# Kernel tuning notes

Hardware: AMD Instinct MI355X
Metric: run time of the kernel (lower is better)

## Reference

```python
import jax, jax.numpy as jnp
import numpy as np

EPS = 1e-9

def dice(x, alpha):
    # Dice: batch-norm over dim 0 (unbiased var, ddof=1), then gated blend.
    mu = jnp.mean(x, axis=0)
    var = jnp.var(x, axis=0, ddof=1)
    p = jax.nn.sigmoid((x - mu) / jnp.sqrt(var + EPS))
    return alpha * x * (1.0 - p) + x * p


def setup_inputs() -> dict:
    key = jax.random.key(0)
    ks = jax.random.split(key, 8)
    bs, seq, dim = 2048, 200, 64
    d_in = dim * 4
    return {
        "query": jax.random.normal(ks[0], (bs, dim), jnp.float32),
        "user_behavior": jax.random.normal(ks[1], (bs, seq, dim), jnp.float32),
        "mask": jax.random.uniform(ks[2], (bs, seq, 1), jnp.float32),
        "W1": jax.random.normal(ks[3], (d_in, 32), jnp.float32) / np.sqrt(d_in),
        "b1": jnp.zeros((32,), jnp.float32),
        "alpha1": jnp.zeros((1,), jnp.float32),
        "W2": jax.random.normal(ks[4], (32, 16), jnp.float32) / np.sqrt(32.0),
        "b2": jnp.zeros((16,), jnp.float32),
        "alpha2": jnp.zeros((1,), jnp.float32),
        "W3": jax.random.normal(ks[5], (16, 1), jnp.float32) / np.sqrt(16.0),
        "b3": jnp.zeros((1,), jnp.float32),
    }


def reference(query, user_behavior, mask, W1, b1, alpha1, W2, b2, alpha2, W3, b3):
    # query: (bs, dim) -> broadcast to (bs, seq, dim)
    q = jnp.broadcast_to(query[:, None, :], user_behavior.shape)
    attn_input = jnp.concatenate(
        [q, user_behavior, q - user_behavior, q * user_behavior], axis=-1
    )  # (bs, seq, 4*dim)
    h = dice(attn_input @ W1 + b1, alpha1)
    h = dice(h @ W2 + b2, alpha2)
    attns = h @ W3 + b3  # (bs, seq, 1)
    attns = attns * mask
    output = jnp.sum(user_behavior * attns, axis=1)  # (bs, dim)
    return output, attns
```

## Files before the change

kernel.cpp:

```cpp
#include <hip/hip_runtime.h>
#include <math.h>

#define BS  2048
#define SEQ 200
#define DIM 64
#define C1  32
#define C2  16

__device__ __forceinline__ float dice1(float x, float m, float r, float al) {
    float t = (x - m) * r;
    float p = 1.f / (1.f + __expf(-t));
    return x * (al + p * (1.f - al));
}

__global__ __launch_bounds__(256) void k_fold(const float* __restrict__ W1,
                                              float* __restrict__ Wq,
                                              float* __restrict__ Wu,
                                              float* __restrict__ Wp) {
    int i = blockIdx.x * 256 + threadIdx.x;
    if (i < DIM * C1) {
        float a = W1[i];
        float b = W1[DIM * C1 + i];
        float c = W1[2 * DIM * C1 + i];
        float d = W1[3 * DIM * C1 + i];
        Wq[i] = a + c;
        Wu[i] = b - c;
        Wp[i] = d;
    }
}

__global__ __launch_bounds__(256) void k_gemm1(const float* __restrict__ q,
                                               const float* __restrict__ ub,
                                               const float* __restrict__ Wq,
                                               const float* __restrict__ Wu,
                                               const float* __restrict__ Wp,
                                               const float* __restrict__ b1,
                                               float* __restrict__ z1) {
    const int bs = blockIdx.x;
    const int tid = threadIdx.x;
    __shared__ float s_q[DIM];
    __shared__ __align__(16) float s_qw[C1];
    __shared__ __align__(16) float s_wc[DIM * C1];
    __shared__ float s_ub[32 * 65];

    if (tid < DIM) s_q[tid] = q[bs * DIM + tid];
    __syncthreads();
    for (int i = tid; i < DIM * C1; i += 256)
        s_wc[i] = Wu[i] + s_q[i >> 5] * Wp[i];
    if (tid < C1) {
        float a = b1[tid];
        #pragma unroll
        for (int d = 0; d < DIM; ++d) a = fmaf(s_q[d], Wq[(d << 5) + tid], a);
        s_qw[tid] = a;
    }

    const float4* wc4 = (const float4*)s_wc;
    const int sl = tid >> 3;
    const int cq = tid & 7;
    const float* ub_b = ub + (size_t)bs * SEQ * DIM;
    float* z1_b = z1 + (size_t)bs * SEQ * C1;

    for (int s0 = 0; s0 < SEQ; s0 += 32) {
        const int cn = min(32, SEQ - s0);
        const float4* src = (const float4*)(ub_b + s0 * DIM);
        const int nf4 = cn * 16;
        __syncthreads();
        for (int i = tid; i < nf4; i += 256) {
            float4 v = src[i];
            int f = i * 4;
            int r = f >> 6, d = f & 63;
            float* dst = &s_ub[r * 65 + d];
            dst[0] = v.x; dst[1] = v.y; dst[2] = v.z; dst[3] = v.w;
        }
        __syncthreads();
        if (sl < cn) {
            float4 acc;
            acc.x = s_qw[cq * 4 + 0];
            acc.y = s_qw[cq * 4 + 1];
            acc.z = s_qw[cq * 4 + 2];
            acc.w = s_qw[cq * 4 + 3];
            const float* urow = &s_ub[sl * 65];
            #pragma unroll 16
            for (int d = 0; d < DIM; ++d) {
                float u = urow[d];
                float4 w = wc4[(d << 3) + cq];
                acc.x = fmaf(u, w.x, acc.x);
                acc.y = fmaf(u, w.y, acc.y);
                acc.z = fmaf(u, w.z, acc.z);
                acc.w = fmaf(u, w.w, acc.w);
            }
            ((float4*)(z1_b + (s0 + sl) * C1))[cq] = acc;
        }
    }
}

template <int C>
__global__ __launch_bounds__(1024) void k_red(const float* __restrict__ z,
                                              float* __restrict__ mu,
                                              float* __restrict__ rstd) {
    const int seq = blockIdx.x;
    const int tid = threadIdx.x;
    const int c = tid % C;
    const int g = tid / C;
    const int NG = 1024 / C;
    float s = 0.f, ss = 0.f;
    for (int b = g; b < BS; b += NG) {
        float v = z[((size_t)b * SEQ + seq) * C + c];
        s += v;
        ss = fmaf(v, v, ss);
    }
    __shared__ float sh_s[1024], sh_ss[1024];
    sh_s[tid] = s;
    sh_ss[tid] = ss;
    __syncthreads();
    if (tid < C) {
        float ts = 0.f, tss = 0.f;
        for (int g2 = 0; g2 < NG; ++g2) {
            ts += sh_s[g2 * C + c];
            tss += sh_ss[g2 * C + c];
        }
        float m = ts / (float)BS;
        float var = (tss - ts * m) / (float)(BS - 1);
        mu[seq * C + c] = m;
        rstd[seq * C + c] = rsqrtf(var + 1e-9f);
    }
}

__global__ __launch_bounds__(256) void k_gemm2(const float* __restrict__ z1,
                                               const float* __restrict__ mu1,
                                               const float* __restrict__ rstd1,
                                               const float* __restrict__ alpha1,
                                               const float* __restrict__ W2,
                                               const float* __restrict__ b2,
                                               float* __restrict__ z2) {
    const int bs = blockIdx.x;
    const int tid = threadIdx.x;
    __shared__ __align__(16) float s_w2[C1 * C2];
    __shared__ float s_b2[C2];
    for (int i = tid; i < C1 * C2; i += 256) s_w2[i] = W2[i];
    if (tid < C2) s_b2[tid] = b2[tid];
    __syncthreads();
    if (tid >= SEQ) return;
    const float al = alpha1[0];
    const int seq = tid;
    const float4* z4 = (const float4*)(z1 + ((size_t)bs * SEQ + seq) * C1);
    const float4* m4 = (const float4*)(mu1 + seq * C1);
    const float4* r4 = (const float4*)(rstd1 + seq * C1);
    float h[C1];
    #pragma unroll
    for (int k = 0; k < C1 / 4; ++k) {
        float4 x = z4[k], m = m4[k], r = r4[k];
        h[k * 4 + 0] = dice1(x.x, m.x, r.x, al);
        h[k * 4 + 1] = dice1(x.y, m.y, r.y, al);
        h[k * 4 + 2] = dice1(x.z, m.z, r.z, al);
        h[k * 4 + 3] = dice1(x.w, m.w, r.w, al);
    }
    const float4* w4 = (const float4*)s_w2;
    float4 o[4];
    #pragma unroll
    for (int qd = 0; qd < 4; ++qd) {
        o[qd].x = s_b2[qd * 4 + 0];
        o[qd].y = s_b2[qd * 4 + 1];
        o[qd].z = s_b2[qd * 4 + 2];
        o[qd].w = s_b2[qd * 4 + 3];
    }
    #pragma unroll
    for (int c = 0; c < C1; ++c) {
        float hc = h[c];
        #pragma unroll
        for (int qd = 0; qd < 4; ++qd) {
            float4 w = w4[c * 4 + qd];
            o[qd].x = fmaf(hc, w.x, o[qd].x);
            o[qd].y = fmaf(hc, w.y, o[qd].y);
            o[qd].z = fmaf(hc, w.z, o[qd].z);
            o[qd].w = fmaf(hc, w.w, o[qd].w);
        }
    }
    float4* outp = (float4*)(z2 + ((size_t)bs * SEQ + seq) * C2);
    #pragma unroll
    for (int qd = 0; qd < 4; ++qd) outp[qd] = o[qd];
}

__global__ __launch_bounds__(256) void k_final(const float* __restrict__ z2,
                                               const float* __restrict__ mu2,
                                               const float* __restrict__ rstd2,
                                               const float* __restrict__ alpha2,
                                               const float* __restrict__ W3,
                                               const float* __restrict__ b3,
                                               const float* __restrict__ mask,
                                               const float* __restrict__ ub,
                                               float* __restrict__ out,
                                               float* __restrict__ attns) {
    const int bs = blockIdx.x;
    const int tid = threadIdx.x;
    __shared__ float s_attn[SEQ];
    __shared__ float s_w3[C2];
    __shared__ float s_part[4][DIM];
    if (tid < C2) s_w3[tid] = W3[tid];
    __syncthreads();
    if (tid < SEQ) {
        const float al = alpha2[0];
        const float bb3 = b3[0];
        const int seq = tid;
        const float4* z4 = (const float4*)(z2 + ((size_t)bs * SEQ + seq) * C2);
        const float4* m4 = (const float4*)(mu2 + seq * C2);
        const float4* r4 = (const float4*)(rstd2 + seq * C2);
        float a = bb3;
        #pragma unroll
        for (int k = 0; k < C2 / 4; ++k) {
            float4 x = z4[k], m = m4[k], r = r4[k];
            a = fmaf(dice1(x.x, m.x, r.x, al), s_w3[k * 4 + 0], a);
            a = fmaf(dice1(x.y, m.y, r.y, al), s_w3[k * 4 + 1], a);
            a = fmaf(dice1(x.z, m.z, r.z, al), s_w3[k * 4 + 2], a);
            a = fmaf(dice1(x.w, m.w, r.w, al), s_w3[k * 4 + 3], a);
        }
        a *= mask[bs * SEQ + seq];
        s_attn[seq] = a;
        attns[(size_t)bs * SEQ + seq] = a;
    }
    __syncthreads();
    const int d = tid & 63;
    const int sg = tid >> 6;
    float acc = 0.f;
    const float* ub_b = ub + (size_t)bs * SEQ * DIM;
    for (int s = sg; s < SEQ; s += 4)
        acc = fmaf(ub_b[s * DIM + d], s_attn[s], acc);
    s_part[sg][d] = acc;
    __syncthreads();
    if (tid < DIM) {
        float r = s_part[0][tid] + s_part[1][tid] + s_part[2][tid] + s_part[3][tid];
        out[(size_t)bs * DIM + tid] = r;
    }
}

extern "C" void kernel_launch(void* const* d_in, const int* in_sizes, int n_in,
                              void* d_out, int out_size, void* d_ws, size_t ws_size,
                              hipStream_t stream) {
    const float* q    = (const float*)d_in[0];
    const float* ub   = (const float*)d_in[1];
    const float* mask = (const float*)d_in[2];
    const float* W1   = (const float*)d_in[3];
    const float* b1   = (const float*)d_in[4];
    const float* a1   = (const float*)d_in[5];
    const float* W2   = (const float*)d_in[6];
    const float* b2   = (const float*)d_in[7];
    const float* a2   = (const float*)d_in[8];
    const float* W3   = (const float*)d_in[9];
    const float* b3   = (const float*)d_in[10];

    float* out   = (float*)d_out;
    float* attns = out + (size_t)BS * DIM;

    float* ws = (float*)d_ws;
    float* Wq = ws;
    float* Wu = Wq + 2048;
    float* Wp = Wu + 2048;
    float* z1 = Wp + 2048;
    float* z2 = z1 + (size_t)BS * SEQ * C1;
    float* mu1   = z2 + (size_t)BS * SEQ * C2;
    float* rstd1 = mu1 + SEQ * C1;
    float* mu2   = rstd1 + SEQ * C1;
    float* rstd2 = mu2 + SEQ * C2;

    hipLaunchKernelGGL(k_fold, dim3(8), dim3(256), 0, stream, W1, Wq, Wu, Wp);
    hipLaunchKernelGGL(k_gemm1, dim3(BS), dim3(256), 0, stream, q, ub, Wq, Wu, Wp, b1, z1);
    hipLaunchKernelGGL((k_red<C1>), dim3(SEQ), dim3(1024), 0, stream, z1, mu1, rstd1);
    hipLaunchKernelGGL(k_gemm2, dim3(BS), dim3(256), 0, stream, z1, mu1, rstd1, a1, W2, b2, z2);
    hipLaunchKernelGGL((k_red<C2>), dim3(SEQ), dim3(1024), 0, stream, z2, mu2, rstd2);
    hipLaunchKernelGGL(k_final, dim3(BS), dim3(256), 0, stream, z2, mu2, rstd2, a2, W3, b3, mask, ub, out, attns);
}
```

Measured before the change: 299.1 us.

## Fold W1 inside gemm1, stage full sequence in LDS, vectorize reductions

Removes the separate weight-fold kernel and folds W1 slices directly inside gemm1. gemm1 now loads the whole 200-row user_behavior tile into padded LDS with float4 stores in one pass, and each thread computes 7 rows with register accumulators instead of looping over 32-row chunks with repeated barriers. The batch-norm reduction kernel reads float4 and uses a tree reduction in shared memory. This cuts one launch, reduces syncs and raises ILP, at the cost of about 54KB of LDS per block, which limits occupancy.

```diff
diff --git a/kernel.cpp b/kernel.cpp
--- a/kernel.cpp
+++ b/kernel.cpp
@@ -6,6 +6,7 @@
 #define DIM 64
 #define C1  32
 #define C2  16
+#define PAD 68
 
 __device__ __forceinline__ float dice1(float x, float m, float r, float al) {
     float t = (x - m) * r;
@@ -13,84 +14,78 @@
     return x * (al + p * (1.f - al));
 }
 
-__global__ __launch_bounds__(256) void k_fold(const float* __restrict__ W1,
-                                              float* __restrict__ Wq,
-                                              float* __restrict__ Wu,
-                                              float* __restrict__ Wp) {
-    int i = blockIdx.x * 256 + threadIdx.x;
-    if (i < DIM * C1) {
-        float a = W1[i];
-        float b = W1[DIM * C1 + i];
-        float c = W1[2 * DIM * C1 + i];
-        float d = W1[3 * DIM * C1 + i];
-        Wq[i] = a + c;
-        Wu[i] = b - c;
-        Wp[i] = d;
-    }
-}
-
 __global__ __launch_bounds__(256) void k_gemm1(const float* __restrict__ q,
                                                const float* __restrict__ ub,
-                                               const float* __restrict__ Wq,
-                                               const float* __restrict__ Wu,
-                                               const float* __restrict__ Wp,
+                                               const float* __restrict__ W1,
                                                const float* __restrict__ b1,
                                                float* __restrict__ z1) {
     const int bs = blockIdx.x;
     const int tid = threadIdx.x;
-    __shared__ float s_q[DIM];
+    __shared__ __align__(16) float s_ub[SEQ * PAD];
+    __shared__ __align__(16) float s_wc[DIM * C1];
     __shared__ __align__(16) float s_qw[C1];
-    __shared__ __align__(16) float s_wc[DIM * C1];
-    __shared__ float s_ub[32 * 65];
-
-    if (tid < DIM) s_q[tid] = q[bs * DIM + tid];
-    __syncthreads();
-    for (int i = tid; i < DIM * C1; i += 256)
-        s_wc[i] = Wu[i] + s_q[i >> 5] * Wp[i];
+
+    float4* s_ub4 = (float4*)s_ub;
+    const float4* s_wc4 = (const float4*)s_wc;
+    const float* qrow = q + bs * DIM;
+    const float* ub_b = ub + (size_t)bs * SEQ * DIM;
+
+    const float4* src4 = (const float4*)ub_b;
+    for (int t = tid; t < SEQ * 16; t += 256)
+        s_ub4[(t >> 4) * 17 + (t & 15)] = src4[t];
+
+    const float4* w1b4 = (const float4*)(W1 + DIM * C1);
+    const float4* w1c4 = (const float4*)(W1 + 2 * DIM * C1);
+    const float4* w1d4 = (const float4*)(W1 + 3 * DIM * C1);
+    for (int i4 = tid; i4 < DIM * C1 / 4; i4 += 256) {
+        int d = i4 >> 3;
+        float qd = qrow[d];
+        float4 bb = w1b4[i4], cc = w1c4[i4], dd = w1d4[i4];
+        float4 r;
+        r.x = bb.x - cc.x + qd * dd.x;
+        r.y = bb.y - cc.y + qd * dd.y;
+        r.z = bb.z - cc.z + qd * dd.z;
+        r.w = bb.w - cc.w + qd * dd.w;
+        ((float4*)s_wc)[i4] = r;
+    }
     if (tid < C1) {
         float a = b1[tid];
-        #pragma unroll
-        for (int d = 0; d < DIM; ++d) a = fmaf(s_q[d], Wq[(d << 5) + tid], a);
+        #pragma unroll 8
+        for (int d = 0; d < DIM; ++d)
+            a = fmaf(qrow[d], W1[(d << 5) + tid] + W1[2 * DIM * C1 + (d << 5) + tid], a);
         s_qw[tid] = a;
     }
-
-    const float4* wc4 = (const float4*)s_wc;
+    __syncthreads();
+
     const int sl = tid >> 3;
     const int cq = tid & 7;
-    const float* ub_b = ub + (size_t)bs * SEQ * DIM;
+    const float4 qw = ((const float4*)s_qw)[cq];
+    const float* su[7];
+    float4 acc[7];
+    #pragma unroll
+    for (int i = 0; i < 7; ++i) {
+        int r = sl + 32 * i;
+        if (r > SEQ - 1) r = SEQ - 1;
+        su[i] = s_ub + r * PAD;
+        acc[i] = qw;
+    }
+    #pragma unroll 4
+    for (int d = 0; d < DIM; ++d) {
+        float4 w = s_wc4[(d << 3) + cq];
+        #pragma unroll
+        for (int i = 0; i < 7; ++i) {
+            float u = su[i][d];
+            acc[i].x = fmaf(u, w.x, acc[i].x);
+            acc[i].y = fmaf(u, w.y, acc[i].y);
+            acc[i].z = fmaf(u, w.z, acc[i].z);
+            acc[i].w = fmaf(u, w.w, acc[i].w);
+        }
+    }
     float* z1_b = z1 + (size_t)bs * SEQ * C1;
-
-    for (int s0 = 0; s0 < SEQ; s0 += 32) {
-        const int cn = min(32, SEQ - s0);
-        const float4* src = (const float4*)(ub_b + s0 * DIM);
-        const int nf4 = cn * 16;
-        __syncthreads();
-        for (int i = tid; i < nf4; i += 256) {
-            float4 v = src[i];
-            int f = i * 4;
-            int r = f >> 6, d = f & 63;
-            float* dst = &s_ub[r * 65 + d];
-            dst[0] = v.x; dst[1] = v.y; dst[2] = v.z; dst[3] = v.w;
-        }
-        __syncthreads();
-        if (sl < cn) {
-            float4 acc;
-            acc.x = s_qw[cq * 4 + 0];
-            acc.y = s_qw[cq * 4 + 1];
-            acc.z = s_qw[cq * 4 + 2];
-            acc.w = s_qw[cq * 4 + 3];
-            const float* urow = &s_ub[sl * 65];
-            #pragma unroll 16
-            for (int d = 0; d < DIM; ++d) {
-                float u = urow[d];
-                float4 w = wc4[(d << 3) + cq];
-                acc.x = fmaf(u, w.x, acc.x);
-                acc.y = fmaf(u, w.y, acc.y);
-                acc.z = fmaf(u, w.z, acc.z);
-                acc.w = fmaf(u, w.w, acc.w);
-            }
-            ((float4*)(z1_b + (s0 + sl) * C1))[cq] = acc;
-        }
+    #pragma unroll
+    for (int i = 0; i < 7; ++i) {
+        int s = sl + 32 * i;
+        if (s < SEQ) ((float4*)(z1_b + s * C1))[cq] = acc[i];
     }
 }
 
@@ -98,31 +93,46 @@
 __global__ __launch_bounds__(1024) void k_red(const float* __restrict__ z,
                                               float* __restrict__ mu,
                                               float* __restrict__ rstd) {
+    constexpr int Q = C / 4;
+    constexpr int NG = 1024 / Q;
     const int seq = blockIdx.x;
-    const int tid = threadIdx.x;
-    const int c = tid % C;
-    const int g = tid / C;
-    const int NG = 1024 / C;
-    float s = 0.f, ss = 0.f;
+    const int cq = threadIdx.x % Q;
+    const int g = threadIdx.x / Q;
+    float4 s = {0.f, 0.f, 0.f, 0.f}, ss = {0.f, 0.f, 0.f, 0.f};
     for (int b = g; b < BS; b += NG) {
-        float v = z[((size_t)b * SEQ + seq) * C + c];
-        s += v;
-        ss = fmaf(v, v, ss);
-    }
-    __shared__ float sh_s[1024], sh_ss[1024];
-    sh_s[tid] = s;
-    sh_ss[tid] = ss;
-    __syncthreads();
-    if (tid < C) {
-        float ts = 0.f, tss = 0.f;
-        for (int g2 = 0; g2 < NG; ++g2) {
-            ts += sh_s[g2 * C + c];
-            tss += sh_ss[g2 * C + c];
-        }
-        float m = ts / (float)BS;
-        float var = (tss - ts * m) / (float)(BS - 1);
-        mu[seq * C + c] = m;
-        rstd[seq * C + c] = rsqrtf(var + 1e-9f);
+        float4 v = *(const float4*)(z + ((size_t)b * SEQ + seq) * C + cq * 4);
+        s.x += v.x; s.y += v.y; s.z += v.z; s.w += v.w;
+        ss.x = fmaf(v.x, v.x, ss.x);
+        ss.y = fmaf(v.y, v.y, ss.y);
+        ss.z = fmaf(v.z, v.z, ss.z);
+        ss.w = fmaf(v.w, v.w, ss.w);
+    }
+    __shared__ __align__(16) float4 sh_s[1024];
+    __shared__ __align__(16) float4 sh_ss[1024];
+    sh_s[threadIdx.x] = s;
+    sh_ss[threadIdx.x] = ss;
+    for (int h = NG / 2; h > 0; h >>= 1) {
+        __syncthreads();
+        if (g < h) {
+            int o = threadIdx.x + h * Q;
+            float4 s2 = sh_s[o], ss2 = sh_ss[o];
+            s.x += s2.x; s.y += s2.y; s.z += s2.z; s.w += s2.w;
+            ss.x += ss2.x; ss.y += ss2.y; ss.z += ss2.z; ss.w += ss2.w;
+            sh_s[threadIdx.x] = s;
+            sh_ss[threadIdx.x] = ss;
+        }
+    }
+    if (g == 0) {
+        const float inv_n = 1.f / (float)BS;
+        const float inv_n1 = 1.f / (float)(BS - 1);
+        float4 m, r;
+        m.x = s.x * inv_n; m.y = s.y * inv_n; m.z = s.z * inv_n; m.w = s.w * inv_n;
+        r.x = rsqrtf((ss.x - s.x * m.x) * inv_n1 + 1e-9f);
+        r.y = rsqrtf((ss.y - s.y * m.y) * inv_n1 + 1e-9f);
+        r.z = rsqrtf((ss.z - s.z * m.z) * inv_n1 + 1e-9f);
+        r.w = rsqrtf((ss.w - s.w * m.w) * inv_n1 + 1e-9f);
+        *(float4*)(mu + seq * C + cq * 4) = m;
+        *(float4*)(rstd + seq * C + cq * 4) = r;
     }
 }
 
@@ -252,18 +262,14 @@
     float* attns = out + (size_t)BS * DIM;
 
     float* ws = (float*)d_ws;
-    float* Wq = ws;
-    float* Wu = Wq + 2048;
-    float* Wp = Wu + 2048;
-    float* z1 = Wp + 2048;
+    float* z1 = ws;
     float* z2 = z1 + (size_t)BS * SEQ * C1;
     float* mu1   = z2 + (size_t)BS * SEQ * C2;
     float* rstd1 = mu1 + SEQ * C1;
     float* mu2   = rstd1 + SEQ * C1;
     float* rstd2 = mu2 + SEQ * C2;
 
-    hipLaunchKernelGGL(k_fold, dim3(8), dim3(256), 0, stream, W1, Wq, Wu, Wp);
-    hipLaunchKernelGGL(k_gemm1, dim3(BS), dim3(256), 0, stream, q, ub, Wq, Wu, Wp, b1, z1);
+    hipLaunchKernelGGL(k_gemm1, dim3(BS), dim3(256), 0, stream, q, ub, W1, b1, z1);
     hipLaunchKernelGGL((k_red<C1>), dim3(SEQ), dim3(1024), 0, stream, z1, mu1, rstd1);
     hipLaunchKernelGGL(k_gemm2, dim3(BS), dim3(256), 0, stream, z1, mu1, rstd1, a1, W2, b2, z2);
     hipLaunchKernelGGL((k_red<C2>), dim3(SEQ), dim3(1024), 0, stream, z2, mu2, rstd2);
```

Result: no change. 297.1 us (-0.7%).
